# Kernel optimization log

Hardware: AMD Instinct MI355X
Metric: run time of the kernel (lower is better)

## Reference

```python
import jax, jax.numpy as jnp
import numpy as np

B, C, H, W = 2, 512, 64, 64
S = 2            # scale_factor
HEADS = 8
GROUPS = 32      # assumed GroupNorm groups for group_norm(in_channels)
DK = C // HEADS
SCALE = 1.0 / DK ** 2   # faithful to source: 1/d_k**2
RES = H // S
R = RES * 2 - 1


def setup_inputs() -> dict:
    key = jax.random.key(0)
    ks = jax.random.split(key, 8)
    f = lambda k, shp, s=0.02: jax.random.normal(k, shp, jnp.float32) * s
    return {
        "x": jax.random.normal(ks[0], (B, C, H, W), jnp.float32),
        "q_w": f(ks[1], (C, C, 1, 1)),
        "q_b": jnp.zeros((C,), jnp.float32),
        "kv_w": f(ks[2], (2 * C, C, 1, 1)),
        "kv_b": jnp.zeros((2 * C,), jnp.float32),
        "off1_w": f(ks[3], (C, C, S, S)),
        "off1_b": jnp.zeros((C,), jnp.float32),
        "gn_w": jnp.ones((C,), jnp.float32),
        "gn_b": jnp.zeros((C,), jnp.float32),
        "off2_w": f(ks[4], (2, C, 1, 1)),
        "rpe_table": f(ks[5], (HEADS, R, R), 0.01),
        "proj_w": f(ks[6], (C, C, 1, 1)),
        "proj_b": jnp.zeros((C,), jnp.float32),
    }


def _conv(x, w, b=None, stride=1):
    y = jax.lax.conv_general_dilated(x, w, (stride, stride), 'VALID',
                                     dimension_numbers=('NCHW', 'OIHW', 'NCHW'))
    return y if b is None else y + b[None, :, None, None]


def _group_norm(x, w, b, eps=1e-5):
    n, c, h, wd = x.shape
    xg = x.reshape(n, GROUPS, -1)
    mu = xg.mean(-1, keepdims=True)
    var = xg.var(-1, keepdims=True)
    xg = (xg - mu) * jax.lax.rsqrt(var + eps)
    return xg.reshape(n, c, h, wd) * w[None, :, None, None] + b[None, :, None, None]


def _grid_sample(img, grid):
    # bilinear, align_corners=True; img [B,C,H,W], grid [B,...,2] in (x,y) order
    Bn, Cn, Hn, Wn = img.shape
    gshape = grid.shape[1:-1]
    g = grid.reshape(Bn, -1, 2)
    x = (g[..., 0] + 1.0) * 0.5 * (Wn - 1)
    y = (g[..., 1] + 1.0) * 0.5 * (Hn - 1)
    x0 = jnp.floor(x); y0 = jnp.floor(y)
    wx = (x - x0)[:, None, :]; wy = (y - y0)[:, None, :]
    x0i = jnp.clip(x0.astype(jnp.int32), 0, Wn - 1)
    x1i = jnp.clip(x0i + 1, 0, Wn - 1)
    y0i = jnp.clip(y0.astype(jnp.int32), 0, Hn - 1)
    y1i = jnp.clip(y0i + 1, 0, Hn - 1)
    imf = img.reshape(Bn, Cn, Hn * Wn)
    gat = lambda yi, xi: jnp.take_along_axis(imf, (yi * Wn + xi)[:, None, :], axis=2)
    out = (gat(y0i, x0i) * (1 - wx) * (1 - wy) + gat(y0i, x1i) * wx * (1 - wy)
           + gat(y1i, x0i) * (1 - wx) * wy + gat(y1i, x1i) * wx * wy)
    return out.reshape(Bn, Cn, *gshape)


def _forward(x, q_w, q_b, kv_w, kv_b, off1_w, off1_b, gn_w, gn_b, off2_w,
             rpe_table, proj_w, proj_b):
    l = H * W
    q = _conv(x, q_w, q_b)                                   # [B,C,H,W]
    t = _conv(q, off1_w, off1_b, stride=S)                   # [B,C,h,w]
    t = jax.nn.gelu(_group_norm(t, gn_w, gn_b), approximate=False)
    offset = _conv(t, off2_w).transpose(0, 2, 3, 1)          # [B,h,w,2] (y,x)
    h, w = offset.shape[1], offset.shape[2]
    n = h * w
    # reference points (linspace 0.5..h-0.5, normalized by h-1)
    ry = (jnp.linspace(0.5, h - 0.5, h) / (h - 1.0)) * 2.0 - 1.0
    rx = (jnp.linspace(0.5, w - 0.5, w) / (w - 1.0)) * 2.0 - 1.0
    ref = jnp.stack(jnp.meshgrid(ry, rx, indexing='ij'), -1)  # [h,w,2]
    pos = jnp.clip(offset + ref[None], -1.0, 1.0)             # [B,h,w,2]
    sampled = _grid_sample(x, pos[..., ::-1])                 # [B,C,h,w] (context=x)
    kv = _conv(sampled.reshape(B, C, 1, n), kv_w, kv_b)       # [B,2C,1,n]
    k, v = kv[:, :C], kv[:, C:]
    qf = q.reshape(B * HEADS, DK, l)
    kf = k.reshape(B * HEADS, DK, n)
    vf = v.reshape(B * HEADS, DK, n)
    attn = jnp.einsum('bcm,bcn->bmn', qf, kf) * SCALE         # [B*H, l, n]
    # query grid (arange, normalized by dim-1)
    gy = jnp.arange(H, dtype=jnp.float32) / (H - 1.0) * 2.0 - 1.0
    gx = jnp.arange(W, dtype=jnp.float32) / (W - 1.0) * 2.0 - 1.0
    qg = jnp.stack(jnp.meshgrid(gy, gx, indexing='ij'), -1).reshape(l, 2)
    disp = (qg[None, :, None, :] - pos.reshape(B, 1, n, 2)) * 0.5  # [B,l,n,2]
    rpe = jnp.broadcast_to(rpe_table[None], (B, HEADS, R, R))
    bias = _grid_sample(rpe, disp[..., ::-1])                  # [B,HEADS,l,n]
    attn = jax.nn.softmax(attn + bias.reshape(B * HEADS, l, n), axis=-1)
    out = jnp.einsum('bmn,bcn->bcm', attn, vf).reshape(B, C, H, W)
    return _conv(out, proj_w, proj_b)


def reference(x, q_w, q_b, kv_w, kv_b, off1_w, off1_b, gn_w, gn_b, off2_w,
              rpe_table, proj_w, proj_b):
    return _forward(x, q_w, q_b, kv_w, kv_b, off1_w, off1_b, gn_w, gn_b,
                    off2_w, rpe_table, proj_w, proj_b)
```

## Files before the change

### kernel.cpp

```cpp
#include <hip/hip_runtime.h>
#include <hip/hip_bf16.h>
#include <math.h>

typedef float floatx4 __attribute__((ext_vector_type(4)));
typedef short shortx8 __attribute__((ext_vector_type(8)));
typedef unsigned short ush;

#define NB    2
#define NC    512
#define NL    4096
#define NN    1024
#define NH    8
#define NDK   64
#define NR    63
#define LOG2E 1.44269504f
#define QT_SCALE (1.44269504f/4096.0f)

#define OFF_Q      0u
#define OFF_AO     0u
#define OFF_SMP    2097152u
#define OFF_QT     4194304u
#define OFF_T      6291456u
#define OFF_GS     7340032u
#define OFF_POS    7340160u
#define OFF_KT     7344256u
#define OFF_VV     7868544u
#define OFF_PART   8392832u
#define OFF_TAB2   8392832u

__device__ __forceinline__ ush f2bf(float f) {
    unsigned u = __float_as_uint(f);
    u += 0x7fffu + ((u >> 16) & 1u);
    return (ush)(u >> 16);
}
__device__ __forceinline__ float bf2f(ush h) {
    return __uint_as_float(((unsigned)h) << 16);
}

template<int NP, int BSRC, int OUTMODE>
__global__ __launch_bounds__(256) void gemm_mfma_k(
    const float* __restrict__ A, const void* __restrict__ Bv,
    const float* __restrict__ bias, void* __restrict__ Yv, void* __restrict__ Y2,
    int M, int K, int P, int KS)
{
    __shared__ ush a_hi[128 * 72];
    __shared__ ush b_hi[64 * 72];
    __shared__ ush a_lo[NP == 3 ? 128 * 72 : 64];
    __shared__ ush b_lo[NP == 3 ? 64 * 72 : 64];

    int tid = threadIdx.x;
    int wv = tid >> 6, lane = tid & 63, quad = lane >> 4, l15 = lane & 15;
    int bz = blockIdx.z;
    int b = bz / KS, ks = bz - b * KS;
    int m0 = blockIdx.y * 128, p0 = blockIdx.x * 64;
    int Ksl = K / KS, kbeg = ks * Ksl;

    floatx4 acc[2][4];
    #pragma unroll
    for (int mt = 0; mt < 2; ++mt)
        #pragma unroll
        for (int pt = 0; pt < 4; ++pt) acc[mt][pt] = (floatx4)0.f;

    for (int kc = 0; kc < Ksl; kc += 64) {
        int kg0 = kbeg + kc;
        #pragma unroll
        for (int r = 0; r < 8; ++r) {
            int idx = r * 256 + tid;
            int m = idx >> 4, k4 = (idx & 15) << 2;
            float4 av = *(const float4*)(A + (size_t)(m0 + m) * K + kg0 + k4);
            int o = m * 72 + k4;
            ush h0 = f2bf(av.x), h1 = f2bf(av.y), h2 = f2bf(av.z), h3 = f2bf(av.w);
            a_hi[o] = h0; a_hi[o + 1] = h1; a_hi[o + 2] = h2; a_hi[o + 3] = h3;
            if (NP == 3) {
                a_lo[o]     = f2bf(av.x - bf2f(h0));
                a_lo[o + 1] = f2bf(av.y - bf2f(h1));
                a_lo[o + 2] = f2bf(av.z - bf2f(h2));
                a_lo[o + 3] = f2bf(av.w - bf2f(h3));
            }
        }
        #pragma unroll
        for (int r = 0; r < 8; ++r) {
            int idx = r * 256 + tid;
            int k = idx >> 5, p2 = (idx & 31) << 1;
            float v0, v1;
            if (BSRC == 0) {
                const float* Bp = (const float*)Bv + (size_t)b * K * P;
                float2 t2 = *(const float2*)(Bp + (size_t)(kg0 + k) * P + p0 + p2);
                v0 = t2.x; v1 = t2.y;
            } else if (BSRC == 1) {
                const float* Bp = (const float*)Bv + (size_t)b * NC * NL;
                int kk = kg0 + k;
                int c = kk >> 2, kh = (kk >> 1) & 1, kw = kk & 1;
                int p = p0 + p2;
                int oh = p >> 5, ow = p & 31;
                const float* base = Bp + (size_t)c * NL + (2 * oh + kh) * 64 + kw;
                v0 = base[2 * ow];
                v1 = base[2 * ow + 2];
            } else {
                const ush* Bp = (const ush*)Bv + (size_t)b * K * P;
                unsigned u = *(const unsigned*)(Bp + (size_t)(kg0 + k) * P + p0 + p2);
                v0 = bf2f((ush)(u & 0xffffu));
                v1 = bf2f((ush)(u >> 16));
            }
            ush h0 = f2bf(v0), h1 = f2bf(v1);
            b_hi[p2 * 72 + k] = h0;
            b_hi[(p2 + 1) * 72 + k] = h1;
            if (NP == 3) {
                b_lo[p2 * 72 + k]       = f2bf(v0 - bf2f(h0));
                b_lo[(p2 + 1) * 72 + k] = f2bf(v1 - bf2f(h1));
            }
        }
        __syncthreads();

        shortx8 ah[2][2], al[2][2];
        #pragma unroll
        for (int mt = 0; mt < 2; ++mt)
            #pragma unroll
            for (int kk = 0; kk < 2; ++kk) {
                int o = (wv * 32 + mt * 16 + l15) * 72 + kk * 32 + quad * 8;
                ah[mt][kk] = *(const shortx8*)&a_hi[o];
                if (NP == 3) al[mt][kk] = *(const shortx8*)&a_lo[o];
            }
        #pragma unroll
        for (int pt = 0; pt < 4; ++pt) {
            #pragma unroll
            for (int kk = 0; kk < 2; ++kk) {
                int o = (pt * 16 + l15) * 72 + kk * 32 + quad * 8;
                shortx8 bh = *(const shortx8*)&b_hi[o];
                acc[0][pt] = __builtin_amdgcn_mfma_f32_16x16x32_bf16(ah[0][kk], bh, acc[0][pt], 0, 0, 0);
                acc[1][pt] = __builtin_amdgcn_mfma_f32_16x16x32_bf16(ah[1][kk], bh, acc[1][pt], 0, 0, 0);
                if (NP == 3) {
                    shortx8 bl = *(const shortx8*)&b_lo[o];
                    acc[0][pt] = __builtin_amdgcn_mfma_f32_16x16x32_bf16(ah[0][kk], bl, acc[0][pt], 0, 0, 0);
                    acc[1][pt] = __builtin_amdgcn_mfma_f32_16x16x32_bf16(ah[1][kk], bl, acc[1][pt], 0, 0, 0);
                    acc[0][pt] = __builtin_amdgcn_mfma_f32_16x16x32_bf16(al[0][kk], bh, acc[0][pt], 0, 0, 0);
                    acc[1][pt] = __builtin_amdgcn_mfma_f32_16x16x32_bf16(al[1][kk], bh, acc[1][pt], 0, 0, 0);
                }
            }
        }
        __syncthreads();
    }

    #pragma unroll
    for (int mt = 0; mt < 2; ++mt) {
        #pragma unroll
        for (int reg = 0; reg < 4; ++reg) {
            int m = m0 + wv * 32 + mt * 16 + quad * 4 + reg;
            float bb = (OUTMODE == 2) ? 0.f : bias[m];
            #pragma unroll
            for (int pt = 0; pt < 4; ++pt) {
                int p = p0 + pt * 16 + l15;
                float val = acc[mt][pt][reg] + bb;
                if (OUTMODE == 0) {
                    ((float*)Yv)[(size_t)b * M * P + (size_t)m * P + p] = val;
                } else if (OUTMODE == 2) {
                    ((float*)Yv)[(size_t)(ks * NB + b) * M * P + (size_t)m * P + p] = val;
                } else if (OUTMODE == 3) {
                    ((float*)Yv)[(size_t)b * M * P + (size_t)m * P + p] = val;
                    int h = m >> 6, d = m & 63;
                    ((ush*)Y2)[(((size_t)(b * 8 + h) * 4096) + p) * 64 + d] = f2bf(val * QT_SCALE);
                } else {
                    if (m < 512) {
                        int h = m >> 6, d = m & 63;
                        ((ush*)Yv)[(((size_t)(b * 8 + h) * 1024) + p) * 64 + d] = f2bf(val);
                    } else {
                        int c = m - 512;
                        ((ush*)Y2)[((size_t)(b * 512) + c) * 1024 + p] = f2bf(val);
                    }
                }
            }
        }
    }
}

__global__ __launch_bounds__(256) void reduce_off1_k(const float* __restrict__ part,
                                                     const float* __restrict__ bias,
                                                     float* __restrict__ t)
{
    int i = blockIdx.x * 256 + threadIdx.x;
    float v = part[i] + part[i + 1048576] + part[i + 2097152] + part[i + 3145728];
    t[i] = v + bias[(i >> 10) & 511];
}

__global__ __launch_bounds__(256) void gn_stats_k(const float* __restrict__ T, float* __restrict__ gs)
{
    int bg = blockIdx.x;
    const float* base = T + (size_t)bg * 16384;
    float s = 0.f, ss = 0.f;
    for (int i = threadIdx.x; i < 16384; i += 256) { float v = base[i]; s += v; ss += v * v; }
    #pragma unroll
    for (int off = 32; off >= 1; off >>= 1) { s += __shfl_xor(s, off); ss += __shfl_xor(ss, off); }
    __shared__ float red[8];
    int wv = threadIdx.x >> 6;
    if ((threadIdx.x & 63) == 0) { red[wv * 2] = s; red[wv * 2 + 1] = ss; }
    __syncthreads();
    if (threadIdx.x == 0) {
        float S = red[0] + red[2] + red[4] + red[6];
        float SS = red[1] + red[3] + red[5] + red[7];
        float mu = S / 16384.f;
        float var = SS / 16384.f - mu * mu;
        gs[bg * 2] = mu;
        gs[bg * 2 + 1] = rsqrtf(var + 1e-5f);
    }
}

__global__ __launch_bounds__(256) void gn_gelu_k(float* __restrict__ T, const float* __restrict__ gs,
                                                 const float* __restrict__ gw, const float* __restrict__ gb)
{
    int idx = blockIdx.x * 256 + threadIdx.x;
    int bg = idx >> 14;
    int c = (idx >> 10) & 511;
    float mu = gs[bg * 2], rs = gs[bg * 2 + 1];
    float v = (T[idx] - mu) * rs * gw[c] + gb[c];
    T[idx] = v * 0.5f * (1.f + erff(v * 0.70710678118654752f));
}

__global__ __launch_bounds__(256) void offset_pos_k(const float* __restrict__ T,
                                                    const float* __restrict__ w2,
                                                    float* __restrict__ pos)
{
    int b = blockIdx.x >> 5;
    int og = threadIdx.x & 31;
    int cg = threadIdx.x >> 5;
    int op = ((blockIdx.x & 31) << 5) + og;
    const float* Tb = T + (size_t)b * NC * NN + (size_t)cg * 64 * NN + op;
    float o0 = 0.f, o1 = 0.f;
    #pragma unroll 4
    for (int c = 0; c < 64; ++c) {
        float tv = Tb[(size_t)c * NN];
        o0 += w2[cg * 64 + c] * tv;
        o1 += w2[512 + cg * 64 + c] * tv;
    }
    __shared__ float rs[2][8][32];
    rs[0][cg][og] = o0;
    rs[1][cg][og] = o1;
    __syncthreads();
    if (threadIdx.x < 64) {
        int coord = threadIdx.x >> 5, og2 = threadIdx.x & 31;
        float s = 0.f;
        #pragma unroll
        for (int k = 0; k < 8; ++k) s += rs[coord][k][og2];
        int opf = ((blockIdx.x & 31) << 5) + og2;
        int oh = opf >> 5, ow = opf & 31;
        float ref = (coord == 0) ? ((0.5f + oh) / 31.f * 2.f - 1.f)
                                 : ((0.5f + ow) / 31.f * 2.f - 1.f);
        pos[((size_t)b * 1024 + opf) * 2 + coord] = fminf(fmaxf(s + ref, -1.f), 1.f);
    }
}

__global__ __launch_bounds__(256) void sample_k(const float* __restrict__ x,
                                                const float* __restrict__ pos,
                                                ush* __restrict__ smp)
{
    int idx = blockIdx.x * 256 + threadIdx.x;
    int j = idx & 1023, c = (idx >> 10) & 511, b = idx >> 19;
    float py = pos[(b * 1024 + j) * 2];
    float px = pos[(b * 1024 + j) * 2 + 1];
    float fx = (px + 1.f) * 0.5f * 63.f;
    float fy = (py + 1.f) * 0.5f * 63.f;
    float flx = floorf(fx), fly = floorf(fy);
    float wx = fx - flx, wy = fy - fly;
    int x0 = min(max((int)flx, 0), 63), y0 = min(max((int)fly, 0), 63);
    int x1 = min(x0 + 1, 63),           y1 = min(y0 + 1, 63);
    const float* xb = x + ((size_t)(b * NC + c)) * NL;
    float v00 = xb[y0 * 64 + x0];
    float v01 = xb[y0 * 64 + x1];
    float v10 = xb[y1 * 64 + x0];
    float v11 = xb[y1 * 64 + x1];
    float v = v00 * (1 - wx) * (1 - wy) + v01 * wx * (1 - wy)
            + v10 * (1 - wx) * wy       + v11 * wx * wy;
    smp[idx] = f2bf(v);
}

__global__ __launch_bounds__(256) void tab2_k(const float* __restrict__ rpe,
                                              unsigned* __restrict__ tab2)
{
    int i = blockIdx.x * 256 + threadIdx.x;
    int h = i >> 12, y = (i >> 6) & 63, x = i & 63;
    const float* R = rpe + (size_t)h * 3969;
    float v0 = (y < 63 && x < 63)     ? R[y * 63 + x] * LOG2E : 0.f;
    float v1 = (y < 63 && x + 1 < 63) ? R[y * 63 + x + 1] * LOG2E : 0.f;
    tab2[i] = (unsigned)f2bf(v0) | ((unsigned)f2bf(v1) << 16);
}

__global__ __launch_bounds__(256) void attn_k(
    const ush* __restrict__ qT, const ush* __restrict__ kT,
    const ush* __restrict__ vv, const float* __restrict__ pos,
    const unsigned* __restrict__ tab2, ush* __restrict__ ao)
{
    __shared__ __align__(16) char smem[33792];
    ush*      pa     = (ush*)smem;
    unsigned* tab_s  = (unsigned*)(smem + 9216);
    float*    posj15 = (float*)(smem + 25600);
    float*    obuf   = (float*)smem;

    int bh = blockIdx.y;
    int b = bh >> 3, h = bh & 7;
    int m0 = blockIdx.x * 64;
    int tid = threadIdx.x;
    int wv = tid >> 6, lane = tid & 63, quad = lane >> 4, l15 = lane & 15;

    const ush* qbase = qT + ((size_t)bh * 4096 + m0 + wv * 16 + l15) * 64 + quad * 8;
    shortx8 qf0 = *(const shortx8*)(qbase);
    shortx8 qf1 = *(const shortx8*)(qbase + 32);

    const uint2* tg = (const uint2*)(tab2 + (size_t)h * 4096);
    uint2* tab_s2 = (uint2*)tab_s;
    for (int i = tid; i < 2048; i += 256) tab_s2[i] = tg[i];
    const float* pb = pos + (size_t)b * 2048;
    for (int i = tid; i < 2048; i += 256) posj15[i] = pb[i] * 15.5f;

    float qy15[4], qx15[4];
    #pragma unroll
    for (int reg = 0; reg < 4; ++reg) {
        int mg = m0 + wv * 16 + quad * 4 + reg;
        qy15[reg] = (float)(mg >> 6) * (31.f / 63.f) + 15.5f;
        qx15[reg] = (float)(mg & 63) * (31.f / 63.f) + 15.5f;
    }

    floatx4 o_acc[4], o_sum;
    #pragma unroll
    for (int dt = 0; dt < 4; ++dt) o_acc[dt] = (floatx4)0.f;
    o_sum = (floatx4)0.f;
    shortx8 vone = {16256, 16256, 16256, 16256, 16256, 16256, 16256, 16256};

    __syncthreads();

    const ush* kbase = kT + (size_t)bh * 1024 * 64;
    const ush* vbase = vv + (size_t)(b * 512 + h * 64) * 1024;

    for (int jc = 0; jc < 16; ++jc) {
        int j0 = jc * 64;
        floatx4 sacc[4];
        #pragma unroll
        for (int jt = 0; jt < 4; ++jt) sacc[jt] = (floatx4)0.f;
        #pragma unroll
        for (int jt = 0; jt < 4; ++jt) {
            const ush* kp = kbase + (size_t)(j0 + jt * 16 + l15) * 64 + quad * 8;
            shortx8 kf0 = *(const shortx8*)kp;
            shortx8 kf1 = *(const shortx8*)(kp + 32);
            sacc[jt] = __builtin_amdgcn_mfma_f32_16x16x32_bf16(qf0, kf0, sacc[jt], 0, 0, 0);
            sacc[jt] = __builtin_amdgcn_mfma_f32_16x16x32_bf16(qf1, kf1, sacc[jt], 0, 0, 0);
        }
        #pragma unroll
        for (int jt = 0; jt < 4; ++jt) {
            int j = j0 + jt * 16 + l15;
            float2 pp = *(const float2*)&posj15[j * 2];
            #pragma unroll
            for (int reg = 0; reg < 4; ++reg) {
                float gy = qy15[reg] - pp.x;
                float gx = qx15[reg] - pp.y;
                float fy = floorf(gy), fx = floorf(gx);
                float wy = gy - fy, wx = gx - fx;
                int y0 = min(max((int)fy, 0), 62);
                int x0 = min(max((int)fx, 0), 62);
                unsigned tw0 = tab_s[(y0 << 6) + x0];
                unsigned tw1 = tab_s[(y0 << 6) + 64 + x0];
                float r00 = __uint_as_float(tw0 << 16);
                float r01 = __uint_as_float(tw0 & 0xffff0000u);
                float r10 = __uint_as_float(tw1 << 16);
                float r11 = __uint_as_float(tw1 & 0xffff0000u);
                float bx0 = r00 + wx * (r01 - r00);
                float bx1 = r10 + wx * (r11 - r10);
                float p = exp2f(sacc[jt][reg] + (bx0 + wy * (bx1 - bx0)));
                pa[(wv * 16 + quad * 4 + reg) * 72 + jt * 16 + l15] = f2bf(p);
            }
        }
        const ush* pbase = pa + (wv * 16 + l15) * 72 + quad * 8;
        shortx8 pf0 = *(const shortx8*)pbase;
        shortx8 pf1 = *(const shortx8*)(pbase + 32);
        o_sum = __builtin_amdgcn_mfma_f32_16x16x32_bf16(pf0, vone, o_sum, 0, 0, 0);
        o_sum = __builtin_amdgcn_mfma_f32_16x16x32_bf16(pf1, vone, o_sum, 0, 0, 0);
        #pragma unroll
        for (int dt = 0; dt < 4; ++dt) {
            const ush* vp = vbase + (size_t)(dt * 16 + l15) * 1024 + j0 + quad * 8;
            shortx8 vf0 = *(const shortx8*)vp;
            shortx8 vf1 = *(const shortx8*)(vp + 32);
            o_acc[dt] = __builtin_amdgcn_mfma_f32_16x16x32_bf16(pf0, vf0, o_acc[dt], 0, 0, 0);
            o_acc[dt] = __builtin_amdgcn_mfma_f32_16x16x32_bf16(pf1, vf1, o_acc[dt], 0, 0, 0);
        }
    }

    __syncthreads();
    float inv[4];
    #pragma unroll
    for (int reg = 0; reg < 4; ++reg) inv[reg] = 1.f / o_sum[reg];
    #pragma unroll
    for (int dt = 0; dt < 4; ++dt)
        #pragma unroll
        for (int reg = 0; reg < 4; ++reg)
            obuf[(dt * 16 + l15) * 68 + wv * 16 + quad * 4 + reg] = o_acc[dt][reg] * inv[reg];
    __syncthreads();
    ush* aobase = ao + ((size_t)(b * 512 + h * 64)) * 4096 + m0;
    for (int i = tid; i < 4096; i += 256) {
        int d = i >> 6, m = i & 63;
        aobase[(size_t)d * 4096 + m] = f2bf(obuf[d * 68 + m]);
    }
}

extern "C" void kernel_launch(void* const* d_in, const int* in_sizes, int n_in,
                              void* d_out, int out_size, void* d_ws, size_t ws_size,
                              hipStream_t stream) {
    const float* x      = (const float*)d_in[0];
    const float* q_w    = (const float*)d_in[1];
    const float* q_b    = (const float*)d_in[2];
    const float* kv_w   = (const float*)d_in[3];
    const float* kv_b   = (const float*)d_in[4];
    const float* off1_w = (const float*)d_in[5];
    const float* off1_b = (const float*)d_in[6];
    const float* gn_w   = (const float*)d_in[7];
    const float* gn_b   = (const float*)d_in[8];
    const float* off2_w = (const float*)d_in[9];
    const float* rpe    = (const float*)d_in[10];
    const float* proj_w = (const float*)d_in[11];
    const float* proj_b = (const float*)d_in[12];

    float* ws   = (float*)d_ws;
    float* q    = ws + OFF_Q;
    ush*   ao   = (ush*)(ws + OFF_AO);
    ush*   smp  = (ush*)(ws + OFF_SMP);
    ush*   qT   = (ush*)(ws + OFF_QT);
    float* t    = ws + OFF_T;
    float* gs   = ws + OFF_GS;
    float* pos  = ws + OFF_POS;
    ush*   kT   = (ush*)(ws + OFF_KT);
    ush*   vv   = (ush*)(ws + OFF_VV);
    float* part = ws + OFF_PART;
    unsigned* tab2 = (unsigned*)(ws + OFF_TAB2);
    float* out  = (float*)d_out;

    gemm_mfma_k<3, 0, 3><<<dim3(64, 4, 2), 256, 0, stream>>>(q_w, x, q_b, q, qT, 512, 512, 4096, 1);
    gemm_mfma_k<3, 1, 2><<<dim3(16, 4, 8), 256, 0, stream>>>(off1_w, q, nullptr, part, nullptr, 512, 2048, 1024, 4);
    reduce_off1_k<<<4096, 256, 0, stream>>>(part, off1_b, t);
    gn_stats_k<<<64, 256, 0, stream>>>(t, gs);
    gn_gelu_k<<<4096, 256, 0, stream>>>(t, gs, gn_w, gn_b);
    offset_pos_k<<<64, 256, 0, stream>>>(t, off2_w, pos);
    tab2_k<<<128, 256, 0, stream>>>(rpe, tab2);
    sample_k<<<4096, 256, 0, stream>>>(x, pos, smp);
    gemm_mfma_k<1, 2, 4><<<dim3(16, 8, 2), 256, 0, stream>>>(kv_w, smp, kv_b, kT, vv, 1024, 512, 1024, 1);
    attn_k<<<dim3(64, 16), 256, 0, stream>>>(qT, kT, vv, pos, tab2, ao);
    gemm_mfma_k<1, 2, 0><<<dim3(64, 4, 2), 256, 0, stream>>>(proj_w, ao, proj_b, out, nullptr, 512, 512, 4096, 1);
}
```

Measured before the change: 361.8 us.

## Split attention key range across two wave groups with LDS reduction

The attention block grows from 256 to 512 threads. Two groups of four waves each process half of the 1024 keys for the same 64 queries, and their partial numerators and sums are merged through shared memory before normalisation. The shared-memory copy of scaled positions is dropped, and positions are instead read from global memory and scaled inline. The aim is more waves in flight per block to hide MFMA and gather latency, at the cost of extra barriers, an LDS reduction step and higher shared-memory use per block.

```diff
diff --git a/kernel.cpp b/kernel.cpp
--- a/kernel.cpp
+++ b/kernel.cpp
@@ -283,37 +283,37 @@
     tab2[i] = (unsigned)f2bf(v0) | ((unsigned)f2bf(v1) << 16);
 }
 
-__global__ __launch_bounds__(256) void attn_k(
+__global__ __launch_bounds__(512) void attn_k(
     const ush* __restrict__ qT, const ush* __restrict__ kT,
     const ush* __restrict__ vv, const float* __restrict__ pos,
     const unsigned* __restrict__ tab2, ush* __restrict__ ao)
 {
-    __shared__ __align__(16) char smem[33792];
-    ush*      pa     = (ush*)smem;
-    unsigned* tab_s  = (unsigned*)(smem + 9216);
-    float*    posj15 = (float*)(smem + 25600);
-    float*    obuf   = (float*)smem;
+    __shared__ __align__(16) char smem[34816];
+    ush*      pa    = (ush*)smem;
+    unsigned* tab_s = (unsigned*)(smem + 18432);
+    float*    xbuf  = (float*)smem;
+    float*    obuf  = (float*)smem;
 
     int bh = blockIdx.y;
     int b = bh >> 3, h = bh & 7;
     int m0 = blockIdx.x * 64;
     int tid = threadIdx.x;
     int wv = tid >> 6, lane = tid & 63, quad = lane >> 4, l15 = lane & 15;
-
-    const ush* qbase = qT + ((size_t)bh * 4096 + m0 + wv * 16 + l15) * 64 + quad * 8;
+    int wq  = wv & 3;
+    int grp = wv >> 2;
+
+    const ush* qbase = qT + ((size_t)bh * 4096 + m0 + wq * 16 + l15) * 64 + quad * 8;
     shortx8 qf0 = *(const shortx8*)(qbase);
     shortx8 qf1 = *(const shortx8*)(qbase + 32);
 
     const uint2* tg = (const uint2*)(tab2 + (size_t)h * 4096);
     uint2* tab_s2 = (uint2*)tab_s;
-    for (int i = tid; i < 2048; i += 256) tab_s2[i] = tg[i];
-    const float* pb = pos + (size_t)b * 2048;
-    for (int i = tid; i < 2048; i += 256) posj15[i] = pb[i] * 15.5f;
+    for (int i = tid; i < 2048; i += 512) tab_s2[i] = tg[i];
 
     float qy15[4], qx15[4];
     #pragma unroll
     for (int reg = 0; reg < 4; ++reg) {
-        int mg = m0 + wv * 16 + quad * 4 + reg;
+        int mg = m0 + wq * 16 + quad * 4 + reg;
         qy15[reg] = (float)(mg >> 6) * (31.f / 63.f) + 15.5f;
         qx15[reg] = (float)(mg & 63) * (31.f / 63.f) + 15.5f;
     }
@@ -328,8 +328,10 @@
 
     const ush* kbase = kT + (size_t)bh * 1024 * 64;
     const ush* vbase = vv + (size_t)(b * 512 + h * 64) * 1024;
-
-    for (int jc = 0; jc < 16; ++jc) {
+    const float* pb = pos + (size_t)b * 2048;
+    ush* paw = pa + grp * 4608;
+
+    for (int jc = grp * 8; jc < grp * 8 + 8; ++jc) {
         int j0 = jc * 64;
         floatx4 sacc[4];
         #pragma unroll
@@ -345,11 +347,12 @@
         #pragma unroll
         for (int jt = 0; jt < 4; ++jt) {
             int j = j0 + jt * 16 + l15;
-            float2 pp = *(const float2*)&posj15[j * 2];
+            float2 pr = *(const float2*)(pb + j * 2);
+            float py15 = pr.x * 15.5f, px15 = pr.y * 15.5f;
             #pragma unroll
             for (int reg = 0; reg < 4; ++reg) {
-                float gy = qy15[reg] - pp.x;
-                float gx = qx15[reg] - pp.y;
+                float gy = qy15[reg] - py15;
+                float gx = qx15[reg] - px15;
                 float fy = floorf(gy), fx = floorf(gx);
                 float wy = gy - fy, wx = gx - fx;
                 int y0 = min(max((int)fy, 0), 62);
@@ -363,10 +366,10 @@
                 float bx0 = r00 + wx * (r01 - r00);
                 float bx1 = r10 + wx * (r11 - r10);
                 float p = exp2f(sacc[jt][reg] + (bx0 + wy * (bx1 - bx0)));
-                pa[(wv * 16 + quad * 4 + reg) * 72 + jt * 16 + l15] = f2bf(p);
-            }
-        }
-        const ush* pbase = pa + (wv * 16 + l15) * 72 + quad * 8;
+                paw[(wq * 16 + quad * 4 + reg) * 72 + jt * 16 + l15] = f2bf(p);
+            }
+        }
+        const ush* pbase = paw + (wq * 16 + l15) * 72 + quad * 8;
         shortx8 pf0 = *(const shortx8*)pbase;
         shortx8 pf1 = *(const shortx8*)(pbase + 32);
         o_sum = __builtin_amdgcn_mfma_f32_16x16x32_bf16(pf0, vone, o_sum, 0, 0, 0);
@@ -382,17 +385,42 @@
     }
 
     __syncthreads();
-    float inv[4];
-    #pragma unroll
-    for (int reg = 0; reg < 4; ++reg) inv[reg] = 1.f / o_sum[reg];
-    #pragma unroll
-    for (int dt = 0; dt < 4; ++dt)
-        #pragma unroll
-        for (int reg = 0; reg < 4; ++reg)
-            obuf[(dt * 16 + l15) * 68 + wv * 16 + quad * 4 + reg] = o_acc[dt][reg] * inv[reg];
+    if (grp == 1) {
+        #pragma unroll
+        for (int reg = 0; reg < 4; ++reg) {
+            int row = wq * 16 + quad * 4 + reg;
+            #pragma unroll
+            for (int dt = 0; dt < 4; ++dt)
+                xbuf[row * 65 + dt * 16 + l15] = o_acc[dt][reg];
+            if (l15 == 0) xbuf[row * 65 + 64] = o_sum[reg];
+        }
+    }
+    __syncthreads();
+    if (grp == 0) {
+        #pragma unroll
+        for (int reg = 0; reg < 4; ++reg) {
+            int row = wq * 16 + quad * 4 + reg;
+            #pragma unroll
+            for (int dt = 0; dt < 4; ++dt)
+                o_acc[dt][reg] += xbuf[row * 65 + dt * 16 + l15];
+            o_sum[reg] += xbuf[row * 65 + 64];
+        }
+    }
+    __syncthreads();
+
+    if (grp == 0) {
+        float inv[4];
+        #pragma unroll
+        for (int reg = 0; reg < 4; ++reg) inv[reg] = 1.f / o_sum[reg];
+        #pragma unroll
+        for (int dt = 0; dt < 4; ++dt)
+            #pragma unroll
+            for (int reg = 0; reg < 4; ++reg)
+                obuf[(dt * 16 + l15) * 68 + wq * 16 + quad * 4 + reg] = o_acc[dt][reg] * inv[reg];
+    }
     __syncthreads();
     ush* aobase = ao + ((size_t)(b * 512 + h * 64)) * 4096 + m0;
-    for (int i = tid; i < 4096; i += 256) {
+    for (int i = tid; i < 4096; i += 512) {
         int d = i >> 6, m = i & 63;
         aobase[(size_t)d * 4096 + m] = f2bf(obuf[d * 68 + m]);
     }
@@ -438,6 +466,6 @@
     tab2_k<<<128, 256, 0, stream>>>(rpe, tab2);
     sample_k<<<4096, 256, 0, stream>>>(x, pos, smp);
     gemm_mfma_k<1, 2, 4><<<dim3(16, 8, 2), 256, 0, stream>>>(kv_w, smp, kv_b, kT, vv, 1024, 512, 1024, 1);
-    attn_k<<<dim3(64, 16), 256, 0, stream>>>(qT, kT, vv, pos, tab2, ao);
+    attn_k<<<dim3(64, 16), 512, 0, stream>>>(qT, kT, vv, pos, tab2, ao);
     gemm_mfma_k<1, 2, 0><<<dim3(64, 4, 2), 256, 0, stream>>>(proj_w, ao, proj_b, out, nullptr, 512, 512, 4096, 1);
 }
```

New measurement: 373.0 us. 1.03x slower.

## Prefetch K/V fragments, swizzle RPE table and P tile, drop bias clamps

Applied to the files above, without the earlier changes.

The attention kernel now loads the next chunk's K fragments into registers while the current chunk runs, and issues the V loads before the bias/exp work so global latency is hidden. The RPE table is written XOR-swizzled by row, and the P tile columns are swizzled, to cut LDS bank conflicts. Because each block covers a single query row, the y interpolation terms are hoisted out of the inner loop, and the floor/clamp on coordinates is replaced by truncation, which relies on them being non-negative and in range. Launch bounds now request 4 blocks per CU, and the higher register use from the prefetch buffers may force spills.

```diff
diff --git a/kernel.cpp b/kernel.cpp
--- a/kernel.cpp
+++ b/kernel.cpp
@@ -280,10 +280,11 @@
     const float* R = rpe + (size_t)h * 3969;
     float v0 = (y < 63 && x < 63)     ? R[y * 63 + x] * LOG2E : 0.f;
     float v1 = (y < 63 && x + 1 < 63) ? R[y * 63 + x + 1] * LOG2E : 0.f;
-    tab2[i] = (unsigned)f2bf(v0) | ((unsigned)f2bf(v1) << 16);
-}
-
-__global__ __launch_bounds__(256) void attn_k(
+    int xs = x ^ (y & 31);
+    tab2[(h << 12) + (y << 6) + xs] = (unsigned)f2bf(v0) | ((unsigned)f2bf(v1) << 16);
+}
+
+__global__ __launch_bounds__(256, 4) void attn_k(
     const ush* __restrict__ qT, const ush* __restrict__ kT,
     const ush* __restrict__ vv, const float* __restrict__ pos,
     const unsigned* __restrict__ tab2, ush* __restrict__ ao)
@@ -299,6 +300,8 @@
     int m0 = blockIdx.x * 64;
     int tid = threadIdx.x;
     int wv = tid >> 6, lane = tid & 63, quad = lane >> 4, l15 = lane & 15;
+    int swz = (quad >> 1) & 1;
+    int effq = quad ^ ((l15 >> 3) << 1);
 
     const ush* qbase = qT + ((size_t)bh * 4096 + m0 + wv * 16 + l15) * 64 + quad * 8;
     shortx8 qf0 = *(const shortx8*)(qbase);
@@ -310,13 +313,11 @@
     const float* pb = pos + (size_t)b * 2048;
     for (int i = tid; i < 2048; i += 256) posj15[i] = pb[i] * 15.5f;
 
-    float qy15[4], qx15[4];
-    #pragma unroll
-    for (int reg = 0; reg < 4; ++reg) {
-        int mg = m0 + wv * 16 + quad * 4 + reg;
-        qy15[reg] = (float)(mg >> 6) * (31.f / 63.f) + 15.5f;
-        qx15[reg] = (float)(mg & 63) * (31.f / 63.f) + 15.5f;
-    }
+    float qy = (float)(m0 >> 6) * (31.f / 63.f) + 15.5f;
+    float qx15[4];
+    #pragma unroll
+    for (int reg = 0; reg < 4; ++reg)
+        qx15[reg] = (float)(wv * 16 + quad * 4 + reg) * (31.f / 63.f) + 15.5f;
 
     floatx4 o_acc[4], o_sum;
     #pragma unroll
@@ -324,10 +325,20 @@
     o_sum = (floatx4)0.f;
     shortx8 vone = {16256, 16256, 16256, 16256, 16256, 16256, 16256, 16256};
 
-    __syncthreads();
-
     const ush* kbase = kT + (size_t)bh * 1024 * 64;
     const ush* vbase = vv + (size_t)(b * 512 + h * 64) * 1024;
+
+    shortx8 kf0[4], kf1[4];
+    #pragma unroll
+    for (int jt = 0; jt < 4; ++jt) {
+        const ush* kp = kbase + (size_t)(jt * 16 + l15) * 64 + quad * 8;
+        kf0[jt] = *(const shortx8*)kp;
+        kf1[jt] = *(const shortx8*)(kp + 32);
+    }
+
+    __syncthreads();
+
+    int wrow = wv * 16 + quad * 4;
 
     for (int jc = 0; jc < 16; ++jc) {
         int j0 = jc * 64;
@@ -336,26 +347,41 @@
         for (int jt = 0; jt < 4; ++jt) sacc[jt] = (floatx4)0.f;
         #pragma unroll
         for (int jt = 0; jt < 4; ++jt) {
-            const ush* kp = kbase + (size_t)(j0 + jt * 16 + l15) * 64 + quad * 8;
-            shortx8 kf0 = *(const shortx8*)kp;
-            shortx8 kf1 = *(const shortx8*)(kp + 32);
-            sacc[jt] = __builtin_amdgcn_mfma_f32_16x16x32_bf16(qf0, kf0, sacc[jt], 0, 0, 0);
-            sacc[jt] = __builtin_amdgcn_mfma_f32_16x16x32_bf16(qf1, kf1, sacc[jt], 0, 0, 0);
+            sacc[jt] = __builtin_amdgcn_mfma_f32_16x16x32_bf16(qf0, kf0[jt], sacc[jt], 0, 0, 0);
+            sacc[jt] = __builtin_amdgcn_mfma_f32_16x16x32_bf16(qf1, kf1[jt], sacc[jt], 0, 0, 0);
+        }
+        if (jc < 15) {
+            #pragma unroll
+            for (int jt = 0; jt < 4; ++jt) {
+                const ush* kp = kbase + (size_t)(j0 + 64 + jt * 16 + l15) * 64 + quad * 8;
+                kf0[jt] = *(const shortx8*)kp;
+                kf1[jt] = *(const shortx8*)(kp + 32);
+            }
+        }
+        shortx8 vf[4][2];
+        #pragma unroll
+        for (int dt = 0; dt < 4; ++dt) {
+            const ush* vp = vbase + (size_t)(dt * 16 + l15) * 1024 + j0 + quad * 8;
+            vf[dt][0] = *(const shortx8*)vp;
+            vf[dt][1] = *(const shortx8*)(vp + 32);
         }
         #pragma unroll
         for (int jt = 0; jt < 4; ++jt) {
             int j = j0 + jt * 16 + l15;
             float2 pp = *(const float2*)&posj15[j * 2];
+            float gy = qy - pp.x;
+            int y0 = (int)gy;
+            float wy = gy - (float)y0;
+            int rb0 = (y0 << 6), rs0 = y0 & 31;
+            int rb1 = rb0 + 64,  rs1 = (y0 + 1) & 31;
+            int colw = ((jt ^ swz) << 4) + l15;
             #pragma unroll
             for (int reg = 0; reg < 4; ++reg) {
-                float gy = qy15[reg] - pp.x;
                 float gx = qx15[reg] - pp.y;
-                float fy = floorf(gy), fx = floorf(gx);
-                float wy = gy - fy, wx = gx - fx;
-                int y0 = min(max((int)fy, 0), 62);
-                int x0 = min(max((int)fx, 0), 62);
-                unsigned tw0 = tab_s[(y0 << 6) + x0];
-                unsigned tw1 = tab_s[(y0 << 6) + 64 + x0];
+                int x0 = (int)gx;
+                float wx = gx - (float)x0;
+                unsigned tw0 = tab_s[rb0 + (x0 ^ rs0)];
+                unsigned tw1 = tab_s[rb1 + (x0 ^ rs1)];
                 float r00 = __uint_as_float(tw0 << 16);
                 float r01 = __uint_as_float(tw0 & 0xffff0000u);
                 float r10 = __uint_as_float(tw1 << 16);
@@ -363,21 +389,18 @@
                 float bx0 = r00 + wx * (r01 - r00);
                 float bx1 = r10 + wx * (r11 - r10);
                 float p = exp2f(sacc[jt][reg] + (bx0 + wy * (bx1 - bx0)));
-                pa[(wv * 16 + quad * 4 + reg) * 72 + jt * 16 + l15] = f2bf(p);
-            }
-        }
-        const ush* pbase = pa + (wv * 16 + l15) * 72 + quad * 8;
+                pa[(wrow + reg) * 72 + colw] = f2bf(p);
+            }
+        }
+        const ush* pbase = pa + (wv * 16 + l15) * 72 + effq * 8;
         shortx8 pf0 = *(const shortx8*)pbase;
         shortx8 pf1 = *(const shortx8*)(pbase + 32);
         o_sum = __builtin_amdgcn_mfma_f32_16x16x32_bf16(pf0, vone, o_sum, 0, 0, 0);
         o_sum = __builtin_amdgcn_mfma_f32_16x16x32_bf16(pf1, vone, o_sum, 0, 0, 0);
         #pragma unroll
         for (int dt = 0; dt < 4; ++dt) {
-            const ush* vp = vbase + (size_t)(dt * 16 + l15) * 1024 + j0 + quad * 8;
-            shortx8 vf0 = *(const shortx8*)vp;
-            shortx8 vf1 = *(const shortx8*)(vp + 32);
-            o_acc[dt] = __builtin_amdgcn_mfma_f32_16x16x32_bf16(pf0, vf0, o_acc[dt], 0, 0, 0);
-            o_acc[dt] = __builtin_amdgcn_mfma_f32_16x16x32_bf16(pf1, vf1, o_acc[dt], 0, 0, 0);
+            o_acc[dt] = __builtin_amdgcn_mfma_f32_16x16x32_bf16(pf0, vf[dt][0], o_acc[dt], 0, 0, 0);
+            o_acc[dt] = __builtin_amdgcn_mfma_f32_16x16x32_bf16(pf1, vf[dt][1], o_acc[dt], 0, 0, 0);
         }
     }
 
```

After: 361.2 us. About the same (-0.2%).
